# Kernel optimization log

Measured on AMD Instinct MI355X. Metric: run time of the kernel, lower is better.

## Reference

```python
import jax, jax.numpy as jnp
import numpy as np

B, L, DM = 32, 64, 512
NODES = 16            # patch_size -> graph nodes
NODE_DIM = 10
CONV_CH, SKIP_CH = 32, 32
GDEP = 2
ALPHA = 0.05
D_STATE, D_CONV = 16, 4
D_INNER = 2 * DM      # Mamba expand=2
DT_RANK = DM // 16    # 32
K = DM - NODES + 1    # start_conv kernel height = 497


def setup_inputs() -> dict:
    key = jax.random.key(0)
    ks = jax.random.split(key, 16)
    n = jax.random.normal
    inp = {
        "x": n(ks[0], (B, L, DM), jnp.float32),
        "nodevec1": n(ks[1], (NODES, NODE_DIM), jnp.float32),
        "nodevec2": n(ks[2], (NODE_DIM, NODES), jnp.float32),
        "start_w": n(ks[3], (CONV_CH, K), jnp.float32) * 0.02,
        "start_b": jnp.zeros((CONV_CH,), jnp.float32),
        "mix_w": n(ks[4], (SKIP_CH, (GDEP + 1) * CONV_CH), jnp.float32) * 0.05,
        "mix_b": jnp.zeros((SKIP_CH,), jnp.float32),
        "end_w": n(ks[5], (L, SKIP_CH, L), jnp.float32) * 0.02,
        "end_b": jnp.zeros((L,), jnp.float32),
        "lin_w": n(ks[6], (DM, NODES), jnp.float32) * 0.05,
        "lin_b": jnp.zeros((DM,), jnp.float32),
        "gnorm_g": jnp.ones((DM,), jnp.float32),
        "gnorm_b": jnp.zeros((DM,), jnp.float32),
        "in_proj_w": n(ks[7], (2 * D_INNER, DM), jnp.float32) * 0.02,
        "conv_w": n(ks[8], (D_INNER, D_CONV), jnp.float32) * 0.2,
        "conv_b": jnp.zeros((D_INNER,), jnp.float32),
        "xproj_w": n(ks[9], (DT_RANK + 2 * D_STATE, D_INNER), jnp.float32) * 0.02,
        "dtproj_w": n(ks[10], (D_INNER, DT_RANK), jnp.float32) * 0.05,
        "dtproj_b": n(ks[11], (D_INNER,), jnp.float32) * 0.05,
        "A_log": jnp.log(jnp.tile(jnp.arange(1, D_STATE + 1, dtype=jnp.float32), (D_INNER, 1))),
        "Dp": jnp.ones((D_INNER,), jnp.float32),
        "out_proj_w": n(ks[12], (DM, D_INNER), jnp.float32) * 0.02,
        "norm_g": jnp.ones((DM,), jnp.float32),
        "norm_b": jnp.zeros((DM,), jnp.float32),
    }
    return inp


def layer_norm(x, g, b, eps=1e-5):
    mu = x.mean(-1, keepdims=True)
    var = ((x - mu) ** 2).mean(-1, keepdims=True)
    return (x - mu) / jnp.sqrt(var + eps) * g + b


def graph_block(x, nodevec1, nodevec2, start_w, start_b, mix_w, mix_b,
                end_w, end_b, lin_w, lin_b, gnorm_g, gnorm_b):
    # adaptive adjacency over the NODES=16 graph nodes
    adp = jax.nn.softmax(jax.nn.relu(nodevec1 @ nodevec2), axis=1)
    # start_conv: Conv2d(1, CONV_CH, (DM-NODES+1, 1)) on [B,1,DM,L]
    xi = jnp.swapaxes(x, 1, 2)  # [B, DM, L]
    windows = jnp.stack([xi[:, i:i + K, :] for i in range(NODES)], axis=1)  # [B, NODES, K, L]
    h0 = jnp.einsum('bikl,ck->bcil', windows, start_w) + start_b[None, :, None, None]  # [B,CONV_CH,NODES,L]
    # mixprop graph conv
    adj = adp + jnp.eye(NODES, dtype=x.dtype)
    a = adj / adj.sum(axis=1, keepdims=True)
    h = h0
    outs = [h]
    for _ in range(GDEP):
        h = ALPHA * h0 + (1.0 - ALPHA) * jnp.einsum('bcwl,vw->bcvl', h, a)
        outs.append(h)
    ho = jnp.concatenate(outs, axis=1)  # [B, (GDEP+1)*CONV_CH, NODES, L]
    ho = jnp.einsum('bcil,oc->boil', ho, mix_w) + mix_b[None, :, None, None]  # 1x1 conv mlp
    ho = jax.nn.gelu(ho, approximate=False)
    # end_conv: Conv2d(SKIP_CH, L, (1, L)) -> [B, L, NODES]
    out = jnp.einsum('bcil,ocl->boi', ho, end_w) + end_b[None, :, None]
    out = out @ lin_w.T + lin_b  # [B, L, DM]
    return layer_norm(x + out, gnorm_g, gnorm_b)


def mamba(x, in_proj_w, conv_w, conv_b, xproj_w, dtproj_w, dtproj_b,
          A_log, Dp, out_proj_w):
    xz = x @ in_proj_w.T                       # [B,L,2*D_INNER]
    xin, z = jnp.split(xz, 2, axis=-1)
    # causal depthwise conv1d
    xt = jnp.swapaxes(xin, 1, 2)               # [B, D_INNER, L]
    xp = jnp.pad(xt, ((0, 0), (0, 0), (D_CONV - 1, 0)))
    xc = sum(xp[:, :, k:k + L] * conv_w[None, :, k, None] for k in range(D_CONV))
    xc = xc + conv_b[None, :, None]
    xc = jax.nn.silu(jnp.swapaxes(xc, 1, 2))   # [B, L, D_INNER]
    x_dbl = xc @ xproj_w.T
    dt, Bm, Cm = jnp.split(x_dbl, [DT_RANK, DT_RANK + D_STATE], axis=-1)
    dt = jax.nn.softplus(dt @ dtproj_w.T + dtproj_b)      # [B,L,D_INNER]
    A = -jnp.exp(A_log)                                    # [D_INNER, D_STATE]
    dA = jnp.exp(dt[..., None] * A)                        # [B,L,D_INNER,D_STATE]
    dBu = dt[..., None] * Bm[:, :, None, :] * xc[..., None]

    def step(h, inputs):
        dA_t, dBu_t, C_t = inputs
        h = dA_t * h + dBu_t                               # [B,D_INNER,D_STATE]
        y = jnp.einsum('bds,bs->bd', h, C_t)
        return h, y

    h0 = jnp.zeros((B, D_INNER, D_STATE), dtype=x.dtype)
    _, ys = jax.lax.scan(step, h0, (jnp.swapaxes(dA, 0, 1),
                                    jnp.swapaxes(dBu, 0, 1),
                                    jnp.swapaxes(Cm, 0, 1)))
    y = jnp.swapaxes(ys, 0, 1) + xc * Dp                   # skip term D*u
    y = y * jax.nn.silu(z)
    return y @ out_proj_w.T


def reference(x, nodevec1, nodevec2, start_w, start_b, mix_w, mix_b, end_w, end_b,
              lin_w, lin_b, gnorm_g, gnorm_b, in_proj_w, conv_w, conv_b, xproj_w,
              dtproj_w, dtproj_b, A_log, Dp, out_proj_w, norm_g, norm_b):
    xg = graph_block(x, nodevec1, nodevec2, start_w, start_b, mix_w, mix_b,
                     end_w, end_b, lin_w, lin_b, gnorm_g, gnorm_b)
    out = layer_norm(mamba(xg, in_proj_w, conv_w, conv_b, xproj_w, dtproj_w,
                           dtproj_b, A_log, Dp, out_proj_w), norm_g, norm_b)
    out = jax.nn.gelu(out, approximate=False)
    return out + xg
```

## Files before the change

### kernel.cpp

```cpp
#include <hip/hip_runtime.h>
#include <hip/hip_bf16.h>
#include <math.h>

typedef __hip_bfloat16 bf16;
typedef __attribute__((ext_vector_type(8))) short short8;
typedef __attribute__((ext_vector_type(4))) float f32x4;

#define B_ 32
#define L_ 64
#define DM_ 512
#define NODES_ 16
#define KW_ 497
#define DIN_ 1024

__device__ __forceinline__ float b2f(bf16 x){ return __bfloat162float(x); }
__device__ __forceinline__ bf16 f2b(float x){ return __float2bfloat16(x); }
__device__ __forceinline__ float us2f(unsigned short u){ return __uint_as_float(((unsigned)u)<<16); }
__device__ __forceinline__ float geluf(float x){ return 0.5f*x*(1.0f+erff(x*0.70710678118654752f)); }
__device__ __forceinline__ float siluf(float x){ return x/(1.0f+__expf(-x)); }

__global__ void k_prep(const float* nv1, const float* nv2, float* a_out,
                       const float* ew, bf16* ewt, const float* win, bf16* wbin,
                       const float* wo, bf16* wob, const float* xw, bf16* xwt,
                       const float* dw, float* dwt){
  int bid = blockIdx.x;
  if (bid < 512){
    int idx = bid*256 + threadIdx.x;
    int o = idx >> 11, j = idx & 2047;
    int c = j & 31, l = j >> 5;
    ewt[idx] = f2b(ew[o*2048 + c*64 + l]);
  } else if (bid < 4608){
    int idx = (bid-512)*256 + threadIdx.x;
    wbin[idx] = f2b(win[idx]);
  } else if (bid < 6656){
    int idx = (bid-4608)*256 + threadIdx.x;
    wob[idx] = f2b(wo[idx]);
  } else if (bid < 6912){
    int k = (bid-6656)*256 + threadIdx.x;
    xwt[k] = f2b(xw[(k & 63)*1024 + (k >> 6)]);
  } else if (bid < 7040){
    int k = (bid-6912)*256 + threadIdx.x;
    dwt[k] = dw[(k & 1023)*32 + (k >> 10)];
  } else {
    int i = threadIdx.x;
    if (i >= NODES_) return;
    float row[NODES_];
    for (int j=0;j<NODES_;j++){
      float s = 0.f;
      for (int k=0;k<10;k++) s += nv1[i*10+k] * nv2[k*NODES_+j];
      row[j] = fmaxf(s, 0.f);
    }
    float m = row[0];
    for (int j=1;j<NODES_;j++) m = fmaxf(m,row[j]);
    float den = 0.f;
    for (int j=0;j<NODES_;j++){ row[j] = __expf(row[j]-m); den += row[j]; }
    for (int j=0;j<NODES_;j++) row[j] /= den;
    row[i] += 1.f;
    float rs = 0.f;
    for (int j=0;j<NODES_;j++) rs += row[j];
    float inv = 1.f/rs;
    for (int j=0;j<NODES_;j++) a_out[i*NODES_+j] = row[j]*inv;
  }
}

__global__ void __launch_bounds__(256) k_startconv(const float* x, const float* sw, const float* sb, bf16* hm){
  __shared__ float wsm[16*KW_];
  __shared__ float xs[4][520];
  int tid = threadIdx.x;
  int tok0 = (blockIdx.x >> 1)*4;
  int ch0  = (blockIdx.x & 1)*16;
  for (int t = tid; t < 16*KW_; t += 256) wsm[t] = sw[ch0*KW_ + t];
  for (int t = tid; t < 4*DM_; t += 256){
    int tt = t >> 9, d = t & 511;
    xs[tt][d] = x[(tok0+tt)*DM_ + d];
  }
  if (tid < 32){ int tt = tid>>3; xs[tt][512 + (tid&7)] = 0.f; }
  __syncthreads();
  int sub = tid >> 6;
  int t6  = tid & 63;
  int cl  = t6 >> 2;
  int iq  = t6 & 3;
  const float* xp = &xs[sub][iq*4];
  float a0=0.f,a1=0.f,a2=0.f,a3=0.f;
  float x0 = xp[0], x1 = xp[1], x2 = xp[2], x3 = xp[3];
  const float* wrow = wsm + cl*KW_;
  for (int k=0;k<KW_;k++){
    float w = wrow[k];
    a0 += w*x0; a1 += w*x1; a2 += w*x2; a3 += w*x3;
    x0 = x1; x1 = x2; x2 = x3; x3 = xp[k+4];
  }
  int c = ch0 + cl;
  float bias = sb[c];
  int tok = tok0 + sub;
  bf16* o = hm + tok*512 + c*16 + iq*4;
  o[0]=f2b(a0+bias); o[1]=f2b(a1+bias); o[2]=f2b(a2+bias); o[3]=f2b(a3+bias);
}

__global__ void __launch_bounds__(512) k_mixprop(bf16* hm, const float* a, const float* mw, const float* mb){
  __shared__ float h0s[512], h1s[512], h2s[512], as[256], mws[32*96];
  int tid = threadIdx.x;
  int tok = blockIdx.x;
  h0s[tid] = b2f(hm[tok*512 + tid]);
  if (tid < 256) as[tid] = a[tid];
  for (int t = tid; t < 32*96; t += 512) mws[t] = mw[t];
  __syncthreads();
  int c = tid >> 4, i = tid & 15;
  float s = 0.f;
  for (int w=0;w<16;w++) s += as[i*16+w]*h0s[c*16+w];
  h1s[tid] = 0.05f*h0s[tid] + 0.95f*s;
  __syncthreads();
  float s2 = 0.f;
  for (int w=0;w<16;w++) s2 += as[i*16+w]*h1s[c*16+w];
  h2s[tid] = 0.05f*h0s[tid] + 0.95f*s2;
  __syncthreads();
  int o  = tid & 31, i2 = tid >> 5;
  float acc = mb[o];
  for (int cc=0; cc<32; cc++){
    acc += h0s[cc*16+i2]*mws[o*96+cc]
         + h1s[cc*16+i2]*mws[o*96+32+cc]
         + h2s[cc*16+i2]*mws[o*96+64+cc];
  }
  hm[tok*512 + i2*32 + o] = f2b(geluf(acc));
}

__global__ void k_endconv(const bf16* mixed, const bf16* ewt, const float* eb, float* eout){
  __shared__ float ms[2048];
  __shared__ float psum[64][4];
  int bi = blockIdx.x;
  int b = bi >> 4, i = bi & 15;
  int tid = threadIdx.x;
  {
    int t0 = tid*8;
    int l = t0 >> 5, cc0 = t0 & 31;
    short8 v = *(const short8*)(mixed + (size_t)(b*64+l)*512 + i*32 + cc0);
    #pragma unroll
    for (int k=0;k<8;k++) ms[t0+k] = us2f((unsigned short)v[k]);
  }
  __syncthreads();
  int o = tid >> 2, q = tid & 3;
  const short8* er8 = (const short8*)(ewt + (size_t)o*2048 + q*512);
  const float* mr = ms + q*512;
  float p0 = 0.f, p1 = 0.f;
  for (int j8=0;j8<64;j8++){
    short8 w8 = er8[j8];
    const float* mq = mr + j8*8;
    p0 += mq[0]*us2f((unsigned short)w8[0]) + mq[1]*us2f((unsigned short)w8[1])
        + mq[2]*us2f((unsigned short)w8[2]) + mq[3]*us2f((unsigned short)w8[3]);
    p1 += mq[4]*us2f((unsigned short)w8[4]) + mq[5]*us2f((unsigned short)w8[5])
        + mq[6]*us2f((unsigned short)w8[6]) + mq[7]*us2f((unsigned short)w8[7]);
  }
  psum[o][q] = p0 + p1;
  __syncthreads();
  if (tid < 64){
    float s = psum[tid][0]+psum[tid][1]+psum[tid][2]+psum[tid][3] + eb[tid];
    eout[(b*64+tid)*16 + i] = s;
  }
}

__global__ void __launch_bounds__(512) k_linln(const float* eout, const float* x, const float* lw, const float* lb,
                        const float* gg, const float* gb, bf16* xgb){
  __shared__ float es[16];
  __shared__ float red[8];
  int tok = blockIdx.x;
  int tid = threadIdx.x;
  if (tid < 16) es[tid] = eout[tok*16 + tid];
  __syncthreads();
  float v = x[tok*512+tid] + lb[tid];
  for (int i=0;i<16;i++) v += es[i]*lw[tid*16+i];
  float s = v;
  for (int off=32; off; off>>=1) s += __shfl_down(s, off, 64);
  int wv = tid>>6, ln = tid&63;
  if (ln==0) red[wv] = s;
  __syncthreads();
  if (tid==0){ float t=0.f; for(int w=0;w<8;w++) t+=red[w]; red[0]=t; }
  __syncthreads();
  float mean = red[0] * (1.f/512.f);
  __syncthreads();
  float d = v - mean;
  float s2 = d*d;
  for (int off=32; off; off>>=1) s2 += __shfl_down(s2, off, 64);
  if (ln==0) red[wv] = s2;
  __syncthreads();
  if (tid==0){ float t=0.f; for(int w=0;w<8;w++) t+=red[w]; red[0]=t; }
  __syncthreads();
  float rstd = rsqrtf(red[0]*(1.f/512.f) + 1e-5f);
  xgb[tok*512+tid] = f2b(d*rstd*gg[tid] + gb[tid]);
}

__global__ void __launch_bounds__(256) k_gemm(const ushort* A, int lda,
                                              const ushort* W, int ldw,
                                              int K, bf16* C){
  __shared__ ushort As[128*56] __attribute__((aligned(16)));
  __shared__ ushort Ws[128*56] __attribute__((aligned(16)));
  int tid = threadIdx.x;
  int m0 = blockIdx.y*128, n0 = blockIdx.x*128;
  int lane = tid & 63, wave = tid >> 6;
  int wm = (wave>>1)*64, wn = (wave&1)*64;
  int l15 = lane & 15, quad = lane >> 4;
  f32x4 acc[4][4];
  #pragma unroll
  for (int mi=0;mi<4;mi++)
    #pragma unroll
    for (int ni=0;ni<4;ni++) acc[mi][ni] = (f32x4){0.f,0.f,0.f,0.f};
  for (int k0 = 0; k0 < K; k0 += 32){
    __syncthreads();
    #pragma unroll
    for (int p=0;p<2;p++){
      int idx = p*256 + tid;
      int row = idx>>2, ch = idx&3;
      *(uint4*)&As[row*56 + ch*8] = *(const uint4*)(A + (size_t)(m0+row)*lda + k0 + ch*8);
      *(uint4*)&Ws[row*56 + ch*8] = *(const uint4*)(W + (size_t)(n0+row)*ldw + k0 + ch*8);
    }
    __syncthreads();
    short8 af[4], bfr[4];
    #pragma unroll
    for (int mi=0;mi<4;mi++) af[mi] = *(const short8*)&As[(wm+mi*16+l15)*56 + quad*8];
    #pragma unroll
    for (int ni=0;ni<4;ni++) bfr[ni] = *(const short8*)&Ws[(wn+ni*16+l15)*56 + quad*8];
    #pragma unroll
    for (int mi=0;mi<4;mi++)
      #pragma unroll
      for (int ni=0;ni<4;ni++)
        acc[mi][ni] = __builtin_amdgcn_mfma_f32_16x16x32_bf16(af[mi], bfr[ni], acc[mi][ni], 0, 0, 0);
  }
  #pragma unroll
  for (int mi=0;mi<4;mi++){
    #pragma unroll
    for (int ni=0;ni<4;ni++){
      int col = n0 + wn + ni*16 + l15;
      #pragma unroll
      for (int r=0;r<4;r++){
        int row = m0 + wm + mi*16 + quad*4 + r;
        C[(size_t)row*2048 + col] = f2b(acc[mi][ni][r]);
      }
    }
  }
}

__global__ void __launch_bounds__(256) k_gemm64(const ushort* A, int lda,
                                                const ushort* W, int ldw,
                                                int K, char* Cb){
  __shared__ ushort As[64*56] __attribute__((aligned(16)));
  __shared__ ushort Ws[64*56] __attribute__((aligned(16)));
  int tid = threadIdx.x;
  int m0 = blockIdx.y*64, n0 = blockIdx.x*64;
  int lane = tid & 63, wave = tid >> 6;
  int wm = (wave>>1)*32, wn = (wave&1)*32;
  int l15 = lane & 15, quad = lane >> 4;
  f32x4 acc[2][2];
  #pragma unroll
  for (int mi=0;mi<2;mi++)
    #pragma unroll
    for (int ni=0;ni<2;ni++) acc[mi][ni] = (f32x4){0.f,0.f,0.f,0.f};
  for (int k0 = 0; k0 < K; k0 += 32){
    __syncthreads();
    int row = tid>>2, ch = tid&3;
    *(uint4*)&As[row*56 + ch*8] = *(const uint4*)(A + (size_t)(m0+row)*lda + k0 + ch*8);
    *(uint4*)&Ws[row*56 + ch*8] = *(const uint4*)(W + (size_t)(n0+row)*ldw + k0 + ch*8);
    __syncthreads();
    short8 af[2], bfr[2];
    #pragma unroll
    for (int mi=0;mi<2;mi++) af[mi] = *(const short8*)&As[(wm+mi*16+l15)*56 + quad*8];
    #pragma unroll
    for (int ni=0;ni<2;ni++) bfr[ni] = *(const short8*)&Ws[(wn+ni*16+l15)*56 + quad*8];
    #pragma unroll
    for (int mi=0;mi<2;mi++)
      #pragma unroll
      for (int ni=0;ni<2;ni++)
        acc[mi][ni] = __builtin_amdgcn_mfma_f32_16x16x32_bf16(af[mi], bfr[ni], acc[mi][ni], 0, 0, 0);
  }
  #pragma unroll
  for (int mi=0;mi<2;mi++){
    #pragma unroll
    for (int ni=0;ni<2;ni++){
      int col = n0 + wn + ni*16 + l15;
      #pragma unroll
      for (int r=0;r<4;r++){
        int row = m0 + wm + mi*16 + quad*4 + r;
        *(float*)(Cb + (size_t)row*4096 + col*4) = acc[mi][ni][r];
      }
    }
  }
}

__global__ void __launch_bounds__(256) k_convproj(const bf16* xz, const float* cw, const float* cb,
                          const bf16* xwt, bf16* xcb, float* xdl, float* BC){
  __shared__ float xcs[8*1024];
  __shared__ float ps[8][64][5];
  int tid = threadIdx.x;
  int tok0 = blockIdx.x*8;
  bool first = (tok0 & 63) == 0;
  #pragma unroll
  for (int r = 0; r < 4; r++){
    int j = r*256 + tid;
    float xv[11];
    #pragma unroll
    for (int m=0;m<11;m++){
      int t = tok0 - 3 + m;
      xv[m] = (m < 3 && first) ? 0.f : b2f(xz[(size_t)t*2048 + j]);
    }
    float c0 = cw[j*4+0], c1 = cw[j*4+1], c2 = cw[j*4+2], c3 = cw[j*4+3];
    float cbj = cb[j];
    #pragma unroll
    for (int t=0;t<8;t++){
      float v = cbj + c0*xv[t] + c1*xv[t+1] + c2*xv[t+2] + c3*xv[t+3];
      float xcv = siluf(v);
      xcs[t*1024 + j] = xcv;
      xcb[(size_t)(tok0+t)*1024 + j] = f2b(xcv);
    }
  }
  __syncthreads();
  int e = tid & 63, q = tid >> 6;
  float acc[8];
  #pragma unroll
  for (int t=0;t<8;t++) acc[t]=0.f;
  const bf16* wcol = xwt + (size_t)q*256*64 + e;
  for (int dd=0; dd<256; dd++){
    float w = b2f(wcol[dd*64]);
    #pragma unroll
    for (int t=0;t<8;t++) acc[t] += xcs[t*1024 + q*256 + dd]*w;
  }
  #pragma unroll
  for (int t=0;t<8;t++) ps[t][e][q] = acc[t];
  __syncthreads();
  if (tid < 64){
    int ee = tid;
    for (int t=0;t<8;t++){
      float v = ps[t][ee][0]+ps[t][ee][1]+ps[t][ee][2]+ps[t][ee][3];
      int tok = tok0 + t;
      if (ee < 32) xdl[tok*32 + ee] = v;
      else         BC[tok*32 + (ee-32)] = v;
    }
  }
}

__global__ void __launch_bounds__(128) k_scan5(const float* xdl, const float* BCg,
                       const float* dwt, const float* db, const float* Dp,
                       const bf16* xzz, bf16* xcb){
  __shared__ float bcs[2048];
  __shared__ float xds[2048];
  __shared__ unsigned short xcl[8192];
  __shared__ unsigned short zl[8192];
  int tid = threadIdx.x;
  int b = blockIdx.x >> 3, q = blockIdx.x & 7;
  int d = q*128 + tid;
  for (int t=tid; t<2048; t+=128){ bcs[t] = BCg[b*2048+t]; xds[t] = xdl[b*2048+t]; }
  for (int t=tid; t<8192; t+=128){
    int l = t >> 7, dl = t & 127;
    xcl[t] = ((const unsigned short*)xcb)[(size_t)(b*64+l)*1024 + q*128 + dl];
    zl[t]  = ((const unsigned short*)xzz)[(size_t)(b*64+l)*2048 + 1024 + q*128 + dl];
  }
  float myw[32];
  #pragma unroll
  for (int qq=0;qq<32;qq++) myw[qq] = dwt[qq*1024 + d];
  float dbv = db[d];
  float Dd = Dp[d];
  __syncthreads();
  float h[16];
  #pragma unroll
  for (int s=0;s<16;s++) h[s]=0.f;
  for (int l=0;l<64;l++){
    const float* xr = xds + l*32;
    float a0=dbv, a1=0.f, a2=0.f, a3=0.f;
    #pragma unroll
    for (int j=0;j<8;j++){
      a0 += xr[j]     *myw[j];
      a1 += xr[8+j]   *myw[8+j];
      a2 += xr[16+j]  *myw[16+j];
      a3 += xr[24+j]  *myw[24+j];
    }
    float dtv = (a0+a1)+(a2+a3);
    if (dtv <= 20.f) dtv = __logf(1.f + __expf(dtv));
    float xcv = us2f(xcl[l*128 + tid]);
    float dx = dtv*xcv;
    float e1 = __expf(-dtv);
    float e2 = e1*e1, e4 = e2*e2, e8 = e4*e4;
    float dA[16];
    dA[0]=e1;       dA[1]=e2;       dA[2]=e2*e1;     dA[3]=e4;
    dA[4]=e4*e1;    dA[5]=e4*e2;    dA[6]=e4*dA[2];  dA[7]=e8;
    dA[8]=e8*e1;    dA[9]=e8*e2;    dA[10]=e8*dA[2]; dA[11]=e8*e4;
    dA[12]=e8*dA[4];dA[13]=e8*dA[5];dA[14]=e8*dA[6]; dA[15]=e8*e8;
    const float* bl = bcs + l*32;
    float y0=0.f,y1=0.f,y2=0.f,y3=0.f;
    #pragma unroll
    for (int s=0;s<16;s+=4){
      h[s]   = dA[s]  *h[s]   + dx*bl[s];    y0 += h[s]  *bl[16+s];
      h[s+1] = dA[s+1]*h[s+1] + dx*bl[s+1];  y1 += h[s+1]*bl[17+s];
      h[s+2] = dA[s+2]*h[s+2] + dx*bl[s+2];  y2 += h[s+2]*bl[18+s];
      h[s+3] = dA[s+3]*h[s+3] + dx*bl[s+3];  y3 += h[s+3]*bl[19+s];
    }
    float y = (y0+y1)+(y2+y3);
    float zv = us2f(zl[l*128 + tid]);
    xcb[(size_t)(b*64+l)*1024 + d] = f2b((y + xcv*Dd) * siluf(zv));
  }
}

__global__ void __launch_bounds__(512) k_outfin(const char* ypb, const bf16* xgb,
                        const float* ng, const float* nb, float* out){
  __shared__ float red[8];
  int tok = blockIdx.x, tid = threadIdx.x;
  const float* yr = (const float*)(ypb + (size_t)tok*4096);
  float v = yr[tid];
  float s = v;
  for (int off=32; off; off>>=1) s += __shfl_down(s, off, 64);
  int wv = tid>>6, ln = tid&63;
  if (ln==0) red[wv] = s;
  __syncthreads();
  if (tid==0){ float t=0.f; for(int w=0;w<8;w++) t+=red[w]; red[0]=t; }
  __syncthreads();
  float mean = red[0] * (1.f/512.f);
  __syncthreads();
  float d = v - mean;
  float s2 = d*d;
  for (int off=32; off; off>>=1) s2 += __shfl_down(s2, off, 64);
  if (ln==0) red[wv] = s2;
  __syncthreads();
  if (tid==0){ float t=0.f; for(int w=0;w<8;w++) t+=red[w]; red[0]=t; }
  __syncthreads();
  float rstd = rsqrtf(red[0]*(1.f/512.f) + 1e-5f);
  out[tok*512+tid] = geluf(d*rstd*ng[tid] + nb[tid]) + b2f(xgb[tok*512+tid]);
}

extern "C" void kernel_launch(void* const* d_in, const int* in_sizes, int n_in,
                              void* d_out, int out_size, void* d_ws, size_t ws_size,
                              hipStream_t stream) {
  (void)in_sizes; (void)n_in; (void)out_size; (void)ws_size;
  const float* x        = (const float*)d_in[0];
  const float* nv1      = (const float*)d_in[1];
  const float* nv2      = (const float*)d_in[2];
  const float* start_w  = (const float*)d_in[3];
  const float* start_b  = (const float*)d_in[4];
  const float* mix_w    = (const float*)d_in[5];
  const float* mix_b    = (const float*)d_in[6];
  const float* end_w    = (const float*)d_in[7];
  const float* end_b    = (const float*)d_in[8];
  const float* lin_w    = (const float*)d_in[9];
  const float* lin_b    = (const float*)d_in[10];
  const float* gnorm_g  = (const float*)d_in[11];
  const float* gnorm_b  = (const float*)d_in[12];
  const float* in_proj_w= (const float*)d_in[13];
  const float* conv_w   = (const float*)d_in[14];
  const float* conv_b   = (const float*)d_in[15];
  const float* xproj_w  = (const float*)d_in[16];
  const float* dtproj_w = (const float*)d_in[17];
  const float* dtproj_b = (const float*)d_in[18];
  const float* Dp       = (const float*)d_in[20];
  const float* out_proj_w=(const float*)d_in[21];
  const float* norm_g   = (const float*)d_in[22];
  const float* norm_b   = (const float*)d_in[23];
  float* out = (float*)d_out;

  char* wsb = (char*)d_ws;
  bf16*  xgb   = (bf16*) (wsb + 0);
  bf16*  Wbin  = (bf16*) (wsb + (2u<<20));
  bf16*  Wob   = (bf16*) (wsb + (4u<<20));
  bf16*  xwt   = (bf16*) (wsb + (5u<<20));
  float* dwt   = (float*)(wsb + (5u<<20) + 262144);
  float* xdl   = (float*)(wsb + (6u<<20));
  float* BC    = (float*)(wsb + (6u<<20) + 262144);
  float* a_adj = (float*)(wsb + (7u<<20));
  float* eout  = (float*)(wsb + (7u<<20) + 4096);
  bf16*  ewt   = (bf16*) (wsb + (7u<<20) + 262144);
  bf16*  hm    = (bf16*) (wsb + (8u<<20));
  bf16*  xz    = (bf16*) (wsb + (10u<<20));
  bf16*  xcb   = (bf16*) (wsb + (18u<<20));
  char*  yp    =         (wsb + (22u<<20));

  k_prep     <<<7041, 256, 0, stream>>>(nv1, nv2, a_adj, end_w, ewt, in_proj_w, Wbin,
                                        out_proj_w, Wob, xproj_w, xwt, dtproj_w, dwt);
  k_startconv<<<1024, 256, 0, stream>>>(x, start_w, start_b, hm);
  k_mixprop  <<<2048, 512, 0, stream>>>(hm, a_adj, mix_w, mix_b);
  k_endconv  <<<512,  256, 0, stream>>>(hm, ewt, end_b, eout);
  k_linln    <<<2048, 512, 0, stream>>>(eout, x, lin_w, lin_b, gnorm_g, gnorm_b, xgb);
  k_gemm     <<<dim3(16,16), 256, 0, stream>>>((const ushort*)xgb, 512,
                                               (const ushort*)Wbin, 512,
                                               512, xz);
  k_convproj <<<256,  256, 0, stream>>>(xz, conv_w, conv_b, xwt, xcb, xdl, BC);
  k_scan5    <<<256,  128, 0, stream>>>(xdl, BC, dwt, dtproj_b, Dp, xz, xcb);
  k_gemm64   <<<dim3(8,32), 256, 0, stream>>>((const ushort*)xcb, 1024,
                                              (const ushort*)Wob, 1024,
                                              1024, yp);
  k_outfin   <<<2048, 512, 0, stream>>>(yp, xgb, norm_g, norm_b, out);
}
```

Baseline: 284.0 us.

## Fold start conv and mixprop into one composed weight matrix GEMM

Because the start convolution and graph mix-propagation are both linear per token, they are folded into a single 512x512 weight. This weight is built by multiplying a mixprop matrix Q with a Toeplitz-expanded start-conv weight on MFMA, followed by one bf16 MFMA GEMM with fused bias and GELU. The scalar FP32 start-conv and mixprop kernels go away, and the GEMM kernel is generalised with ldc, bias and activation parameters. It adds weight-composition work on every call, and bf16 rounding of x and of the composed weight adds some precision loss.

```diff
diff --git a/kernel.cpp b/kernel.cpp
--- a/kernel.cpp
+++ b/kernel.cpp
@@ -19,10 +19,10 @@
 __device__ __forceinline__ float geluf(float x){ return 0.5f*x*(1.0f+erff(x*0.70710678118654752f)); }
 __device__ __forceinline__ float siluf(float x){ return x/(1.0f+__expf(-x)); }
 
-__global__ void k_prep(const float* nv1, const float* nv2, float* a_out,
-                       const float* ew, bf16* ewt, const float* win, bf16* wbin,
+__global__ void k_prep(const float* ew, bf16* ewt, const float* win, bf16* wbin,
                        const float* wo, bf16* wob, const float* xw, bf16* xwt,
-                       const float* dw, float* dwt){
+                       const float* dw, float* dwt, const float* x, bf16* xbf,
+                       const float* sw, bf16* SwT){
   int bid = blockIdx.x;
   if (bid < 512){
     int idx = bid*256 + threadIdx.x;
@@ -41,86 +41,119 @@
   } else if (bid < 7040){
     int k = (bid-6912)*256 + threadIdx.x;
     dwt[k] = dw[(k & 1023)*32 + (k >> 10)];
+  } else if (bid < 11136){
+    int idx = (bid-7040)*256 + threadIdx.x;
+    xbf[idx] = f2b(x[idx]);
   } else {
-    int i = threadIdx.x;
-    if (i >= NODES_) return;
-    float row[NODES_];
-    for (int j=0;j<NODES_;j++){
-      float s = 0.f;
-      for (int k=0;k<10;k++) s += nv1[i*10+k] * nv2[k*NODES_+j];
-      row[j] = fmaxf(s, 0.f);
-    }
-    float m = row[0];
-    for (int j=1;j<NODES_;j++) m = fmaxf(m,row[j]);
-    float den = 0.f;
-    for (int j=0;j<NODES_;j++){ row[j] = __expf(row[j]-m); den += row[j]; }
-    for (int j=0;j<NODES_;j++) row[j] /= den;
-    row[i] += 1.f;
-    float rs = 0.f;
-    for (int j=0;j<NODES_;j++) rs += row[j];
-    float inv = 1.f/rs;
-    for (int j=0;j<NODES_;j++) a_out[i*NODES_+j] = row[j]*inv;
-  }
-}
-
-__global__ void __launch_bounds__(256) k_startconv(const float* x, const float* sw, const float* sb, bf16* hm){
-  __shared__ float wsm[16*KW_];
-  __shared__ float xs[4][520];
-  int tid = threadIdx.x;
-  int tok0 = (blockIdx.x >> 1)*4;
-  int ch0  = (blockIdx.x & 1)*16;
-  for (int t = tid; t < 16*KW_; t += 256) wsm[t] = sw[ch0*KW_ + t];
-  for (int t = tid; t < 4*DM_; t += 256){
-    int tt = t >> 9, d = t & 511;
-    xs[tt][d] = x[(tok0+tt)*DM_ + d];
-  }
-  if (tid < 32){ int tt = tid>>3; xs[tt][512 + (tid&7)] = 0.f; }
-  __syncthreads();
-  int sub = tid >> 6;
-  int t6  = tid & 63;
-  int cl  = t6 >> 2;
-  int iq  = t6 & 3;
-  const float* xp = &xs[sub][iq*4];
-  float a0=0.f,a1=0.f,a2=0.f,a3=0.f;
-  float x0 = xp[0], x1 = xp[1], x2 = xp[2], x3 = xp[3];
-  const float* wrow = wsm + cl*KW_;
-  for (int k=0;k<KW_;k++){
-    float w = wrow[k];
-    a0 += w*x0; a1 += w*x1; a2 += w*x2; a3 += w*x3;
-    x0 = x1; x1 = x2; x2 = x3; x3 = xp[k+4];
-  }
-  int c = ch0 + cl;
-  float bias = sb[c];
-  int tok = tok0 + sub;
-  bf16* o = hm + tok*512 + c*16 + iq*4;
-  o[0]=f2b(a0+bias); o[1]=f2b(a1+bias); o[2]=f2b(a2+bias); o[3]=f2b(a3+bias);
-}
-
-__global__ void __launch_bounds__(512) k_mixprop(bf16* hm, const float* a, const float* mw, const float* mb){
-  __shared__ float h0s[512], h1s[512], h2s[512], as[256], mws[32*96];
-  int tid = threadIdx.x;
-  int tok = blockIdx.x;
-  h0s[tid] = b2f(hm[tok*512 + tid]);
-  if (tid < 256) as[tid] = a[tid];
-  for (int t = tid; t < 32*96; t += 512) mws[t] = mw[t];
-  __syncthreads();
-  int c = tid >> 4, i = tid & 15;
-  float s = 0.f;
-  for (int w=0;w<16;w++) s += as[i*16+w]*h0s[c*16+w];
-  h1s[tid] = 0.05f*h0s[tid] + 0.95f*s;
-  __syncthreads();
-  float s2 = 0.f;
-  for (int w=0;w<16;w++) s2 += as[i*16+w]*h1s[c*16+w];
-  h2s[tid] = 0.05f*h0s[tid] + 0.95f*s2;
-  __syncthreads();
-  int o  = tid & 31, i2 = tid >> 5;
-  float acc = mb[o];
-  for (int cc=0; cc<32; cc++){
-    acc += h0s[cc*16+i2]*mws[o*96+cc]
-         + h1s[cc*16+i2]*mws[o*96+32+cc]
-         + h2s[cc*16+i2]*mws[o*96+64+cc];
-  }
-  hm[tok*512 + i2*32 + o] = f2b(geluf(acc));
+    int idx = (bid-11136)*256 + threadIdx.x;
+    int k = idx >> 9, m = idx & 511;
+    int c = m >> 4, w = m & 15;
+    int kk = k - w;
+    SwT[idx] = f2b((kk >= 0 && kk < KW_) ? sw[c*KW_ + kk] : 0.f);
+  }
+}
+
+__global__ void __launch_bounds__(256) k_prepQ(const float* nv1, const float* nv2,
+                        const float* mw, const float* mb, const float* sb,
+                        bf16* Q, float* bcomp){
+  __shared__ float as[256], M1[256], M2[256], mws[32*96], sbs[32], bo[32];
+  int tid = threadIdx.x;
+  for (int t=tid; t<32*96; t+=256) mws[t]=mw[t];
+  if (tid<32) sbs[tid]=sb[tid];
+  __syncthreads();
+  if (tid<16){
+    int i=tid;
+    float row[16];
+    for(int j=0;j<16;j++){ float s=0.f; for(int k=0;k<10;k++) s+=nv1[i*10+k]*nv2[k*16+j]; row[j]=fmaxf(s,0.f); }
+    float m=row[0]; for(int j=1;j<16;j++) m=fmaxf(m,row[j]);
+    float den=0.f; for(int j=0;j<16;j++){row[j]=__expf(row[j]-m); den+=row[j];}
+    for(int j=0;j<16;j++) row[j]/=den;
+    row[i]+=1.f;
+    float rs=0.f; for(int j=0;j<16;j++) rs+=row[j];
+    float inv=1.f/rs;
+    for(int j=0;j<16;j++) as[i*16+j]=row[j]*inv;
+  }
+  __syncthreads();
+  { int i=tid>>4, w=tid&15;
+    M1[tid] = 0.05f*((i==w)?1.f:0.f) + 0.95f*as[i*16+w]; }
+  __syncthreads();
+  { int i=tid>>4, w=tid&15;
+    float s=0.f;
+    for(int u=0;u<16;u++) s+=as[i*16+u]*M1[u*16+w];
+    M2[tid] = 0.05f*((i==w)?1.f:0.f) + 0.95f*s; }
+  if (tid<32){
+    float s=mb[tid];
+    for(int c=0;c<32;c++) s += (mws[tid*96+c]+mws[tid*96+32+c]+mws[tid*96+64+c])*sbs[c];
+    bo[tid]=s;
+  }
+  __syncthreads();
+  if (blockIdx.x == 0){
+    for (int n=tid; n<512; n+=256) bcomp[n] = bo[n&31];
+  }
+  int base = blockIdx.x*4096;
+  for (int t=tid; t<4096; t+=256){
+    int idx = base + t;
+    int n=idx>>9, m=idx&511;
+    int i=n>>5, o=n&31, c=m>>4, w=m&15;
+    float v = mws[o*96+c]*((i==w)?1.f:0.f)
+            + mws[o*96+32+c]*M1[i*16+w]
+            + mws[o*96+64+c]*M2[i*16+w];
+    Q[idx]=f2b(v);
+  }
+}
+
+__global__ void __launch_bounds__(256) k_gemmU(const ushort* A, int lda,
+                                               const ushort* W, int ldw,
+                                               int K, bf16* C, int ldc,
+                                               const float* bias, int act){
+  __shared__ ushort As[128*56] __attribute__((aligned(16)));
+  __shared__ ushort Ws[128*56] __attribute__((aligned(16)));
+  int tid = threadIdx.x;
+  int m0 = blockIdx.y*128, n0 = blockIdx.x*128;
+  int lane = tid & 63, wave = tid >> 6;
+  int wm = (wave>>1)*64, wn = (wave&1)*64;
+  int l15 = lane & 15, quad = lane >> 4;
+  f32x4 acc[4][4];
+  #pragma unroll
+  for (int mi=0;mi<4;mi++)
+    #pragma unroll
+    for (int ni=0;ni<4;ni++) acc[mi][ni] = (f32x4){0.f,0.f,0.f,0.f};
+  for (int k0 = 0; k0 < K; k0 += 32){
+    __syncthreads();
+    #pragma unroll
+    for (int p=0;p<2;p++){
+      int idx = p*256 + tid;
+      int row = idx>>2, ch = idx&3;
+      *(uint4*)&As[row*56 + ch*8] = *(const uint4*)(A + (size_t)(m0+row)*lda + k0 + ch*8);
+      *(uint4*)&Ws[row*56 + ch*8] = *(const uint4*)(W + (size_t)(n0+row)*ldw + k0 + ch*8);
+    }
+    __syncthreads();
+    short8 af[4], bfr[4];
+    #pragma unroll
+    for (int mi=0;mi<4;mi++) af[mi] = *(const short8*)&As[(wm+mi*16+l15)*56 + quad*8];
+    #pragma unroll
+    for (int ni=0;ni<4;ni++) bfr[ni] = *(const short8*)&Ws[(wn+ni*16+l15)*56 + quad*8];
+    #pragma unroll
+    for (int mi=0;mi<4;mi++)
+      #pragma unroll
+      for (int ni=0;ni<4;ni++)
+        acc[mi][ni] = __builtin_amdgcn_mfma_f32_16x16x32_bf16(af[mi], bfr[ni], acc[mi][ni], 0, 0, 0);
+  }
+  #pragma unroll
+  for (int mi=0;mi<4;mi++){
+    #pragma unroll
+    for (int ni=0;ni<4;ni++){
+      int col = n0 + wn + ni*16 + l15;
+      float bs = (act==1) ? bias[col] : 0.f;
+      #pragma unroll
+      for (int r=0;r<4;r++){
+        int row = m0 + wm + mi*16 + quad*4 + r;
+        float v = acc[mi][ni][r];
+        if (act==1) v = geluf(v + bs);
+        C[(size_t)row*ldc + col] = f2b(v);
+      }
+    }
+  }
 }
 
 __global__ void k_endconv(const bf16* mixed, const bf16* ewt, const float* eb, float* eout){
@@ -185,56 +218,6 @@
   __syncthreads();
   float rstd = rsqrtf(red[0]*(1.f/512.f) + 1e-5f);
   xgb[tok*512+tid] = f2b(d*rstd*gg[tid] + gb[tid]);
-}
-
-__global__ void __launch_bounds__(256) k_gemm(const ushort* A, int lda,
-                                              const ushort* W, int ldw,
-                                              int K, bf16* C){
-  __shared__ ushort As[128*56] __attribute__((aligned(16)));
-  __shared__ ushort Ws[128*56] __attribute__((aligned(16)));
-  int tid = threadIdx.x;
-  int m0 = blockIdx.y*128, n0 = blockIdx.x*128;
-  int lane = tid & 63, wave = tid >> 6;
-  int wm = (wave>>1)*64, wn = (wave&1)*64;
-  int l15 = lane & 15, quad = lane >> 4;
-  f32x4 acc[4][4];
-  #pragma unroll
-  for (int mi=0;mi<4;mi++)
-    #pragma unroll
-    for (int ni=0;ni<4;ni++) acc[mi][ni] = (f32x4){0.f,0.f,0.f,0.f};
-  for (int k0 = 0; k0 < K; k0 += 32){
-    __syncthreads();
-    #pragma unroll
-    for (int p=0;p<2;p++){
-      int idx = p*256 + tid;
-      int row = idx>>2, ch = idx&3;
-      *(uint4*)&As[row*56 + ch*8] = *(const uint4*)(A + (size_t)(m0+row)*lda + k0 + ch*8);
-      *(uint4*)&Ws[row*56 + ch*8] = *(const uint4*)(W + (size_t)(n0+row)*ldw + k0 + ch*8);
-    }
-    __syncthreads();
-    short8 af[4], bfr[4];
-    #pragma unroll
-    for (int mi=0;mi<4;mi++) af[mi] = *(const short8*)&As[(wm+mi*16+l15)*56 + quad*8];
-    #pragma unroll
-    for (int ni=0;ni<4;ni++) bfr[ni] = *(const short8*)&Ws[(wn+ni*16+l15)*56 + quad*8];
-    #pragma unroll
-    for (int mi=0;mi<4;mi++)
-      #pragma unroll
-      for (int ni=0;ni<4;ni++)
-        acc[mi][ni] = __builtin_amdgcn_mfma_f32_16x16x32_bf16(af[mi], bfr[ni], acc[mi][ni], 0, 0, 0);
-  }
-  #pragma unroll
-  for (int mi=0;mi<4;mi++){
-    #pragma unroll
-    for (int ni=0;ni<4;ni++){
-      int col = n0 + wn + ni*16 + l15;
-      #pragma unroll
-      for (int r=0;r<4;r++){
-        int row = m0 + wm + mi*16 + quad*4 + r;
-        C[(size_t)row*2048 + col] = f2b(acc[mi][ni][r]);
-      }
-    }
-  }
 }
 
 __global__ void __launch_bounds__(256) k_gemm64(const ushort* A, int lda,
@@ -458,27 +441,33 @@
   float* dwt   = (float*)(wsb + (5u<<20) + 262144);
   float* xdl   = (float*)(wsb + (6u<<20));
   float* BC    = (float*)(wsb + (6u<<20) + 262144);
-  float* a_adj = (float*)(wsb + (7u<<20));
   float* eout  = (float*)(wsb + (7u<<20) + 4096);
   bf16*  ewt   = (bf16*) (wsb + (7u<<20) + 262144);
   bf16*  hm    = (bf16*) (wsb + (8u<<20));
   bf16*  xz    = (bf16*) (wsb + (10u<<20));
   bf16*  xcb   = (bf16*) (wsb + (18u<<20));
   char*  yp    =         (wsb + (22u<<20));
-
-  k_prep     <<<7041, 256, 0, stream>>>(nv1, nv2, a_adj, end_w, ewt, in_proj_w, Wbin,
-                                        out_proj_w, Wob, xproj_w, xwt, dtproj_w, dwt);
-  k_startconv<<<1024, 256, 0, stream>>>(x, start_w, start_b, hm);
-  k_mixprop  <<<2048, 512, 0, stream>>>(hm, a_adj, mix_w, mix_b);
-  k_endconv  <<<512,  256, 0, stream>>>(hm, ewt, end_b, eout);
-  k_linln    <<<2048, 512, 0, stream>>>(eout, x, lin_w, lin_b, gnorm_g, gnorm_b, xgb);
-  k_gemm     <<<dim3(16,16), 256, 0, stream>>>((const ushort*)xgb, 512,
-                                               (const ushort*)Wbin, 512,
-                                               512, xz);
-  k_convproj <<<256,  256, 0, stream>>>(xz, conv_w, conv_b, xwt, xcb, xdl, BC);
-  k_scan5    <<<256,  128, 0, stream>>>(xdl, BC, dwt, dtproj_b, Dp, xz, xcb);
-  k_gemm64   <<<dim3(8,32), 256, 0, stream>>>((const ushort*)xcb, 1024,
-                                              (const ushort*)Wob, 1024,
-                                              1024, yp);
-  k_outfin   <<<2048, 512, 0, stream>>>(yp, xgb, norm_g, norm_b, out);
-}
+  bf16*  xbf   = (bf16*) (wsb + (30u<<20));
+  bf16*  SwT   = (bf16*) (wsb + (32u<<20));
+  bf16*  Q     = (bf16*) (wsb + (33u<<20));
+  bf16*  Wcomp = (bf16*) (wsb + (34u<<20));
+  float* bcomp = (float*)(wsb + (35u<<20));
+
+  k_prep  <<<12160, 256, 0, stream>>>(end_w, ewt, in_proj_w, Wbin, out_proj_w, Wob,
+                                      xproj_w, xwt, dtproj_w, dwt, x, xbf, start_w, SwT);
+  k_prepQ <<<64,    256, 0, stream>>>(nv1, nv2, mix_w, mix_b, start_b, Q, bcomp);
+  k_gemmU <<<dim3(4,4),  256, 0, stream>>>((const ushort*)Q, 512, (const ushort*)SwT, 512,
+                                           512, Wcomp, 512, (const float*)0, 0);
+  k_gemmU <<<dim3(4,16), 256, 0, stream>>>((const ushort*)xbf, 512, (const ushort*)Wcomp, 512,
+                                           512, hm, 512, bcomp, 1);
+  k_endconv<<<512,  256, 0, stream>>>(hm, ewt, end_b, eout);
+  k_linln  <<<2048, 512, 0, stream>>>(eout, x, lin_w, lin_b, gnorm_g, gnorm_b, xgb);
+  k_gemmU  <<<dim3(16,16), 256, 0, stream>>>((const ushort*)xgb, 512, (const ushort*)Wbin, 512,
+                                             512, xz, 2048, (const float*)0, 0);
+  k_convproj<<<256, 256, 0, stream>>>(xz, conv_w, conv_b, xwt, xcb, xdl, BC);
+  k_scan5  <<<256,  128, 0, stream>>>(xdl, BC, dwt, dtproj_b, Dp, xz, xcb);
+  k_gemm64 <<<dim3(8,32), 256, 0, stream>>>((const ushort*)xcb, 1024,
+                                            (const ushort*)Wob, 1024,
+                                            1024, yp);
+  k_outfin <<<2048, 512, 0, stream>>>(yp, xgb, norm_g, norm_b, out);
+}
```

Result: faster. 276.1 us (-2.8%).
